# Optimization experiments

Measured on AMD Instinct MI355X. Metric: run time of the kernel, lower is better.

## Reference

```python
import jax, jax.numpy as jnp
import numpy as np

DIM = 64
K = 8
B_TAIL = 3.0
HIDDEN = 64
BATCH = 16384
MIN_BIN_WIDTH = 1e-3
MIN_BIN_HEIGHT = 1e-3
MIN_DERIVATIVE = 1e-3


def setup_inputs() -> dict:
    key = jax.random.key(0)
    ks = jax.random.split(key, 8)
    L = DIM - 1
    out_dim = 3 * K - 1
    def u(k, shape, fan_in):
        b = 1.0 / np.sqrt(fan_in)
        return jax.random.uniform(k, shape, minval=-b, maxval=b, dtype=jnp.float32)
    return {
        "x": jax.random.normal(ks[0], (BATCH, DIM), jnp.float32),
        "init_param": jax.random.uniform(ks[1], (out_dim,), minval=-0.5, maxval=0.5, dtype=jnp.float32),
        # conditioner MLP i (i=1..dim-1) maps x[:, :i] -> 3K-1; stacked with zero-masked inputs
        "W1": u(ks[2], (L, HIDDEN, DIM), DIM),
        "b1": u(ks[3], (L, HIDDEN), DIM),
        "W2": u(ks[4], (L, HIDDEN, HIDDEN), HIDDEN),
        "b2": u(ks[5], (L, HIDDEN), HIDDEN),
        "W3": u(ks[6], (L, out_dim, HIDDEN), HIDDEN),
        "b3": u(ks[7], (L, out_dim), HIDDEN),
    }


def _rqs(inputs, uW, uH, uD, left, right):
    # inputs: [D, B]; uW/uH: [D, B, K]; uD: [D, B, K+1] (already edge-padded)
    num_bins = uW.shape[-1]
    widths = jax.nn.softmax(uW, axis=-1)
    widths = MIN_BIN_WIDTH + (1 - MIN_BIN_WIDTH * num_bins) * widths
    cw = jnp.pad(jnp.cumsum(widths, axis=-1), ((0, 0), (0, 0), (1, 0)))
    cw = (right - left) * cw + left
    cw = cw.at[..., 0].set(left).at[..., -1].set(right)
    widths = cw[..., 1:] - cw[..., :-1]

    derivs = MIN_DERIVATIVE + jax.nn.softplus(uD)

    heights = jax.nn.softmax(uH, axis=-1)
    heights = MIN_BIN_HEIGHT + (1 - MIN_BIN_HEIGHT * num_bins) * heights
    ch = jnp.pad(jnp.cumsum(heights, axis=-1), ((0, 0), (0, 0), (1, 0)))
    ch = (right - left) * ch + left  # bottom=left, top=right (symmetric box)
    ch = ch.at[..., 0].set(left).at[..., -1].set(right)
    heights = ch[..., 1:] - ch[..., :-1]

    # searchsorted: sum(inputs >= bin_edges) - 1, with eps on last edge
    cw_s = cw.at[..., -1].add(1e-6)
    bin_idx = jnp.sum(inputs[..., None] >= cw_s, axis=-1) - 1
    bin_idx = jnp.clip(bin_idx, 0, num_bins - 1)[..., None]
    take = lambda a: jnp.take_along_axis(a, bin_idx, axis=-1)[..., 0]

    in_cw = take(cw)
    in_w = take(widths)
    in_ch = take(ch)
    in_h = take(heights)
    in_delta = take(heights / widths)
    d_k = take(derivs)
    d_k1 = take(derivs[..., 1:])

    theta = (inputs - in_cw) / in_w
    t1mt = theta * (1 - theta)
    numer = in_h * (in_delta * theta**2 + d_k * t1mt)
    denom = in_delta + (d_k + d_k1 - 2 * in_delta) * t1mt
    outputs = in_ch + numer / denom
    dnum = in_delta**2 * (d_k1 * theta**2 + 2 * in_delta * t1mt + d_k * (1 - theta) ** 2)
    logabsdet = jnp.log(dnum) - 2 * jnp.log(denom)
    return outputs, logabsdet


def _unconstrained_rqs(inputs, uW, uH, uD, tail_bound):
    inside = (inputs >= -tail_bound) & (inputs <= tail_bound)
    const = float(np.log(np.exp(1 - MIN_DERIVATIVE) - 1))
    uD = jnp.pad(uD, ((0, 0), (0, 0), (1, 1)), constant_values=const)
    x_in = jnp.clip(inputs, -tail_bound, tail_bound)
    out, ld = _rqs(x_in, uW, uH, uD, -tail_bound, tail_bound)
    return jnp.where(inside, out, inputs), jnp.where(inside, ld, 0.0)


def reference(x, init_param, W1, b1, W2, b2, W3, b3):
    Bsz = x.shape[0]
    L = DIM - 1
    # row l of mask keeps x[:, :l+1], zeroes the rest -> identical to per-layer x[:, :i]
    mask = jnp.tril(jnp.ones((L, DIM), x.dtype))
    xm = x[None, :, :] * mask[:, None, :]                         # [L, B, D]
    h = jnp.tanh(jnp.einsum('lbd,lhd->lbh', xm, W1) + b1[:, None, :])
    h = jnp.tanh(jnp.einsum('lbh,lgh->lbg', h, W2) + b2[:, None, :])
    out = jnp.einsum('lbh,loh->lbo', h, W3) + b3[:, None, :]      # [L, B, 3K-1]
    params = jnp.concatenate(
        [jnp.broadcast_to(init_param, (1, Bsz, 3 * K - 1)), out], axis=0)  # [D, B, 3K-1]
    W = 2 * B_TAIL * jax.nn.softmax(params[..., :K], axis=-1)
    H = 2 * B_TAIL * jax.nn.softmax(params[..., K:2 * K], axis=-1)
    Dp = jax.nn.softplus(params[..., 2 * K:])
    z_t, ld = _unconstrained_rqs(x.T, W, H, Dp, B_TAIL)           # [D, B]
    return z_t.T, ld.sum(axis=0)
```

## Files before the change

### kernel.cpp

```cpp
#include <hip/hip_runtime.h>

#define BATCH 16384
#define LAYERS 63
#define BM 128
#define XS 72
#define BLOB_BYTES 21504
#define LDS_OFF 8192
#define LDS_BYTES 13312

typedef float f4 __attribute__((ext_vector_type(4)));
typedef short s8 __attribute__((ext_vector_type(8)));
typedef unsigned int u4 __attribute__((ext_vector_type(4)));

#define LOG2E  1.442695041f
#define LN2    0.6931471806f

__device__ __forceinline__ float rcpf(float v) { return __builtin_amdgcn_rcpf(v); }

__device__ __forceinline__ float exp2_hw(float x) {
#if __has_builtin(__builtin_amdgcn_exp2f)
    return __builtin_amdgcn_exp2f(x);
#else
    return exp2f(x);
#endif
}

__device__ __forceinline__ float fast_tanh(float v) {
    float e = exp2_hw(v * (2.f * LOG2E));
    return 1.f - 2.f * rcpf(e + 1.f);
}
__device__ __forceinline__ float deriv_chain(float p) {
    return 1e-3f + LN2 * __log2f(2.f + exp2_hw(p * LOG2E));
}
__device__ __forceinline__ unsigned short f2bf(float f) {
    unsigned int u = __float_as_uint(f);
    u += 0x7fffu + ((u >> 16) & 1u);
    return (unsigned short)(u >> 16);
}
#if __has_builtin(__builtin_amdgcn_cvt_pk_bf16_f32)
__device__ __forceinline__ unsigned pk2(float a, float b) {
    auto r = __builtin_amdgcn_cvt_pk_bf16_f32(a, b);
    return __builtin_bit_cast(unsigned, r);
}
#else
__device__ __forceinline__ unsigned pk2(float a, float b) {
    return (unsigned)f2bf(a) | ((unsigned)f2bf(b) << 16);
}
#endif
__device__ __forceinline__ unsigned long long pack4(float a, float b, float c, float d) {
    return (unsigned long long)pk2(a, b) | ((unsigned long long)pk2(c, d) << 32);
}

__device__ __forceinline__ void rqs_eval(const float* p, float xv, float& zout, float& ldout) {
    const bool inside = (xv >= -3.f) && (xv <= 3.f);
    const float xi = fminf(fmaxf(xv, -3.f), 3.f);

    float wa[8], ha[8];
    {
        float s = 0.f;
        #pragma unroll
        for (int i = 0; i < 8; i++) { wa[i] = exp2_hw(p[i] * LOG2E); s += wa[i]; }
        float inv = 6.f * rcpf(s);
        #pragma unroll
        for (int i = 0; i < 8; i++) wa[i] *= inv;
        s = 0.f;
        #pragma unroll
        for (int i = 0; i < 8; i++) { wa[i] = exp2_hw(wa[i] * LOG2E); s += wa[i]; }
        inv = 0.992f * rcpf(s);
        #pragma unroll
        for (int i = 0; i < 8; i++) wa[i] = 1e-3f + wa[i] * inv;
    }
    {
        float s = 0.f;
        #pragma unroll
        for (int i = 0; i < 8; i++) { ha[i] = exp2_hw(p[8 + i] * LOG2E); s += ha[i]; }
        float inv = 6.f * rcpf(s);
        #pragma unroll
        for (int i = 0; i < 8; i++) ha[i] *= inv;
        s = 0.f;
        #pragma unroll
        for (int i = 0; i < 8; i++) { ha[i] = exp2_hw(ha[i] * LOG2E); s += ha[i]; }
        inv = 0.992f * rcpf(s);
        #pragma unroll
        for (int i = 0; i < 8; i++) ha[i] = 1e-3f + ha[i] * inv;
    }

    float cw[9], ch[9];
    cw[0] = -3.f; ch[0] = -3.f;
    {
        float cs = 0.f, hs = 0.f;
        #pragma unroll
        for (int k = 1; k < 8; k++) {
            cs += wa[k - 1]; cw[k] = 6.f * cs - 3.f;
            hs += ha[k - 1]; ch[k] = 6.f * hs - 3.f;
        }
    }
    cw[8] = 3.f; ch[8] = 3.f;

    int cnt = 0;
    #pragma unroll
    for (int k = 0; k < 8; k++) cnt += (xi >= cw[k]) ? 1 : 0;
    cnt += (xi >= 3.000001f) ? 1 : 0;
    const int bin = min(max(cnt - 1, 0), 7);

    float in_cw = 0.f, in_w = 1.f, in_ch = 0.f, in_h = 1.f;
    float pd0 = 0.f, pd1 = 0.f;
    #pragma unroll
    for (int k = 0; k < 8; k++)
        if (k == bin) {
            in_cw = cw[k]; in_w = cw[k + 1] - cw[k];
            in_ch = ch[k]; in_h = ch[k + 1] - ch[k];
            if (k >= 1) pd0 = p[15 + k];
            if (k <= 6) pd1 = p[16 + k];
        }
    const float dk  = (bin == 0) ? 1.f : deriv_chain(pd0);
    const float dk1 = (bin == 7) ? 1.f : deriv_chain(pd1);

    const float rw    = rcpf(in_w);
    const float delta = in_h * rw;
    const float th    = (xi - in_cw) * rw;
    const float omt = 1.f - th;
    const float t1  = th * omt;
    const float th2 = th * th;
    const float numer = in_h * (delta * th2 + dk * t1);
    const float denom = delta + (dk + dk1 - 2.f * delta) * t1;
    const float rd    = rcpf(denom);
    const float outv  = in_ch + numer * rd;
    const float dnum  = delta * delta * (dk1 * th2 + 2.f * delta * t1 + dk * omt * omt);
    const float ldv = LN2 * __log2f(dnum * rd * rd);

    zout  = inside ? outv : xv;
    ldout = inside ? ldv : 0.f;
}

__global__ __launch_bounds__(256) void prep_kernel(
    const float* __restrict__ x, const float* __restrict__ init_param,
    const float* __restrict__ W1, const float* __restrict__ W2, const float* __restrict__ W3,
    const float* __restrict__ b1, const float* __restrict__ b2, const float* __restrict__ b3,
    unsigned short* __restrict__ x_bf, unsigned char* __restrict__ blobG,
    float* __restrict__ z, float* __restrict__ ld)
{
    const int tid = threadIdx.x;
    if (blockIdx.x < 1024) {
        size_t idx = (size_t)blockIdx.x * 256 + tid;
        f4 v = *(const f4*)&x[idx * 4];
        *(unsigned long long*)&x_bf[idx * 4] = pack4(v[0], v[1], v[2], v[3]);
        return;
    }
    if (blockIdx.x >= 1024 + LAYERS) {
        const int row = (blockIdx.x - 1024 - LAYERS) * 256 + tid;
        float p[23];
        #pragma unroll
        for (int j = 0; j < 23; j++) p[j] = init_param[j];
        float zv, lv;
        rqs_eval(p, x[(size_t)row * 64], zv, lv);
        z[(size_t)row * 64] = zv;
        ld[row] = lv;
        return;
    }
    const int l = blockIdx.x - 1024;
    unsigned char* gb = blobG + (size_t)l * BLOB_BYTES;
    for (int e = tid; e < 1024; e += 256) {
        int m = e >> 9, r = (e >> 3) & 63, j = e & 7;
        const float* src = (m ? W2 : W1) + (size_t)l * 4096 + r * 64 + j * 8;
        unsigned long long lo = pack4(src[0], src[1], src[2], src[3]);
        unsigned long long hi = pack4(src[4], src[5], src[6], src[7]);
        unsigned long long* dst = (unsigned long long*)(gb + m * 8192 + r * 128 + ((j ^ (r & 7)) << 4));
        dst[0] = lo; dst[1] = hi;
    }
    if (tid < 256) {
        int r = tid >> 3, j = tid & 7;
        unsigned long long lo = 0ull, hi = 0ull;
        if (r < 23) {
            const float* src = W3 + (size_t)l * 1472 + r * 64 + j * 8;
            lo = pack4(src[0], src[1], src[2], src[3]);
            hi = pack4(src[4], src[5], src[6], src[7]);
        }
        unsigned long long* dst = (unsigned long long*)(gb + 16384 + r * 128 + ((j ^ (r & 7)) << 4));
        dst[0] = lo; dst[1] = hi;
    }
    if (tid < 64)        *(float*)(gb + 20480 + tid * 4)         = b1[l * 64 + tid];
    else if (tid < 128)  *(float*)(gb + 20736 + (tid - 64) * 4)  = b2[l * 64 + tid - 64];
    else if (tid < 160)  *(float*)(gb + 20992 + (tid - 128) * 4) = (tid - 128 < 23) ? b3[l * 23 + tid - 128] : 0.f;
    else                 { int e = tid - 160; if (e < 96) *(float*)(gb + 21120 + e * 4) = 0.f; }
}

__global__ __launch_bounds__(256, 5) void mlp_rqs_kernel(
    const float* __restrict__ x, const unsigned short* __restrict__ x_bf,
    const unsigned char* __restrict__ blobG,
    float* __restrict__ z, float* __restrict__ ld)
{
    const int l = blockIdx.y, keff = l + 1;
    const int b0 = blockIdx.x * BM;
    const int tid = threadIdx.x;
    const int ln = tid & 63, wv = tid >> 6;
    const int c = ln & 15, q = ln >> 4;
    const int mbase = wv * 32;
    const int c7 = c & 7;

    __shared__ __align__(16) unsigned char blob[LDS_BYTES];
    __shared__ __align__(16) unsigned short Hs[BM * XS];

    unsigned short* W2s = (unsigned short*)blob;
    unsigned short* W3s = (unsigned short*)(blob + 8192);
    const float* b1s = (const float*)(blob + 12288);
    const float* b2s = (const float*)(blob + 12544);
    const float* b3s = (const float*)(blob + 12800);
    float* PsF = (float*)Hs;

    const unsigned char* gblob = blobG + (size_t)l * BLOB_BYTES;

    for (int t = wv; t < 13; t += 4)
        __builtin_amdgcn_global_load_lds(
            (const __attribute__((address_space(1))) void*)(gblob + LDS_OFF + t * 1024 + ln * 16),
            (__attribute__((address_space(3))) void*)(blob + t * 1024 + ln * 16), 16, 0, 0);

    const int ks1 = (keff + 31) >> 5;

    s8 aw1[2][4];
    #pragma unroll
    for (int mt = 0; mt < 4; mt++)
        aw1[0][mt] = *(const s8*)(gblob + (mt * 16 + c) * 128 + ((q ^ c7) << 4));
    if (ks1 == 2) {
        #pragma unroll
        for (int mt = 0; mt < 4; mt++)
            aw1[1][mt] = *(const s8*)(gblob + (mt * 16 + c) * 128 + (((4 + q) ^ c7) << 4));
    }

    u4 B0u, B1u, B2u{}, B3u{};
    {
        const unsigned short* xr = x_bf + (size_t)(b0 + mbase + c) * 64 + q * 8;
        B0u = *(const u4*)xr;  B1u = *(const u4*)(xr + 1024);
        if (ks1 == 2) { B2u = *(const u4*)(xr + 32); B3u = *(const u4*)(xr + 1024 + 32); }
        const int n = keff - ((ks1 - 1) * 32 + q * 8);
        unsigned mk[4];
        #pragma unroll
        for (int i = 0; i < 4; i++) {
            int m = n - 2 * i;
            mk[i] = (m >= 2) ? 0xFFFFFFFFu : ((m == 1) ? 0xFFFFu : 0u);
        }
        if (ks1 == 2) {
            #pragma unroll
            for (int i = 0; i < 4; i++) { B2u[i] &= mk[i]; B3u[i] &= mk[i]; }
        } else {
            #pragma unroll
            for (int i = 0; i < 4; i++) { B0u[i] &= mk[i]; B1u[i] &= mk[i]; }
        }
    }
    const float xv = x[(size_t)(b0 + (tid & 127)) * 64 + keff];

    __syncthreads();

    {
        f4 acc[4][2];
        #pragma unroll
        for (int mt = 0; mt < 4; mt++) {
            f4 bv = *(const f4*)&b1s[mt * 16 + q * 4];
            acc[mt][0] = bv; acc[mt][1] = bv;
        }
        {
            s8 bx0 = __builtin_bit_cast(s8, B0u), bx1 = __builtin_bit_cast(s8, B1u);
            #pragma unroll
            for (int mt = 0; mt < 4; mt++) {
                acc[mt][0] = __builtin_amdgcn_mfma_f32_16x16x32_bf16(aw1[0][mt], bx0, acc[mt][0], 0, 0, 0);
                acc[mt][1] = __builtin_amdgcn_mfma_f32_16x16x32_bf16(aw1[0][mt], bx1, acc[mt][1], 0, 0, 0);
            }
        }
        if (ks1 == 2) {
            s8 bx0 = __builtin_bit_cast(s8, B2u), bx1 = __builtin_bit_cast(s8, B3u);
            #pragma unroll
            for (int mt = 0; mt < 4; mt++) {
                acc[mt][0] = __builtin_amdgcn_mfma_f32_16x16x32_bf16(aw1[1][mt], bx0, acc[mt][0], 0, 0, 0);
                acc[mt][1] = __builtin_amdgcn_mfma_f32_16x16x32_bf16(aw1[1][mt], bx1, acc[mt][1], 0, 0, 0);
            }
        }
        #pragma unroll
        for (int mt = 0; mt < 4; mt++)
            #pragma unroll
            for (int nt = 0; nt < 2; nt++) {
                f4 a = acc[mt][nt];
                unsigned long long w = (unsigned long long)pk2(fast_tanh(a[0]), fast_tanh(a[1]))
                    | ((unsigned long long)pk2(fast_tanh(a[2]), fast_tanh(a[3])) << 32);
                *(unsigned long long*)&Hs[(mbase + nt * 16 + c) * XS + mt * 16 + q * 4] = w;
            }
    }

    {
        f4 acc[4][2];
        #pragma unroll
        for (int mt = 0; mt < 4; mt++) {
            f4 bv = *(const f4*)&b2s[mt * 16 + q * 4];
            acc[mt][0] = bv; acc[mt][1] = bv;
        }
        #pragma unroll
        for (int ks = 0; ks < 2; ks++) {
            s8 bh0 = *(const s8*)&Hs[(mbase + c) * XS + ks * 32 + q * 8];
            s8 bh1 = *(const s8*)&Hs[(mbase + 16 + c) * XS + ks * 32 + q * 8];
            const int sb = ((ks * 4 + q) ^ c7) * 8;
            #pragma unroll
            for (int mt = 0; mt < 4; mt++) {
                s8 aw = *(const s8*)&W2s[(mt * 16 + c) * 64 + sb];
                acc[mt][0] = __builtin_amdgcn_mfma_f32_16x16x32_bf16(aw, bh0, acc[mt][0], 0, 0, 0);
                acc[mt][1] = __builtin_amdgcn_mfma_f32_16x16x32_bf16(aw, bh1, acc[mt][1], 0, 0, 0);
            }
        }
        #pragma unroll
        for (int mt = 0; mt < 4; mt++)
            #pragma unroll
            for (int nt = 0; nt < 2; nt++) {
                f4 a = acc[mt][nt];
                unsigned long long w = (unsigned long long)pk2(fast_tanh(a[0]), fast_tanh(a[1]))
                    | ((unsigned long long)pk2(fast_tanh(a[2]), fast_tanh(a[3])) << 32);
                *(unsigned long long*)&Hs[(mbase + nt * 16 + c) * XS + mt * 16 + q * 4] = w;
            }
    }

    {
        f4 acc3[2][2];
        #pragma unroll
        for (int mt = 0; mt < 2; mt++) {
            f4 bv = *(const f4*)&b3s[mt * 16 + q * 4];
            acc3[mt][0] = bv; acc3[mt][1] = bv;
        }
        #pragma unroll
        for (int ks = 0; ks < 2; ks++) {
            s8 bh0 = *(const s8*)&Hs[(mbase + c) * XS + ks * 32 + q * 8];
            s8 bh1 = *(const s8*)&Hs[(mbase + 16 + c) * XS + ks * 32 + q * 8];
            const int sb = ((ks * 4 + q) ^ c7) * 8;
            #pragma unroll
            for (int mt = 0; mt < 2; mt++) {
                s8 aw = *(const s8*)&W3s[(mt * 16 + c) * 64 + sb];
                acc3[mt][0] = __builtin_amdgcn_mfma_f32_16x16x32_bf16(aw, bh0, acc3[mt][0], 0, 0, 0);
                acc3[mt][1] = __builtin_amdgcn_mfma_f32_16x16x32_bf16(aw, bh1, acc3[mt][1], 0, 0, 0);
            }
        }
        #pragma unroll
        for (int mt = 0; mt < 2; mt++)
            #pragma unroll
            for (int nt = 0; nt < 2; nt++)
                *(f4*)&PsF[(mbase + nt * 16 + c) * 36 + mt * 16 + q * 4] = acc3[mt][nt];
    }
    __syncthreads();

    if (tid < BM) {
        const float* prow = &PsF[tid * 36];
        f4 pv0 = *(const f4*)(prow + 0);
        f4 pv1 = *(const f4*)(prow + 4);
        f4 pv2 = *(const f4*)(prow + 8);
        f4 pv3 = *(const f4*)(prow + 12);

        const bool inside = (xv >= -3.f) && (xv <= 3.f);
        const float xi = fminf(fmaxf(xv, -3.f), 3.f);

        float e[8];
        float s = 0.f;
        #pragma unroll
        for (int i = 0; i < 4; i++) { e[i]     = exp2_hw(pv0[i] * LOG2E); s += e[i]; }
        #pragma unroll
        for (int i = 0; i < 4; i++) { e[4 + i] = exp2_hw(pv1[i] * LOG2E); s += e[4 + i]; }
        float inv2 = (6.f * LOG2E) * rcpf(s);
        float s2 = 0.f;
        #pragma unroll
        for (int i = 0; i < 8; i++) { e[i] = exp2_hw(e[i] * inv2); s2 += e[i]; }
        float inv3 = (6.f * 0.992f) * rcpf(s2);

        float w6k  = 6e-3f + e[0] * inv3;
        float cs   = -3.f + w6k;
        float in_cw = -3.f, in_w = w6k;
        int bin = 0;
        #pragma unroll
        for (int k = 1; k < 8; k++) {
            w6k = 6e-3f + e[k] * inv3;
            const bool ge = (xi >= cs);
            in_cw = ge ? cs  : in_cw;
            in_w  = ge ? w6k : in_w;
            bin   = ge ? k   : bin;
            cs += w6k;
        }

        s = 0.f;
        #pragma unroll
        for (int i = 0; i < 4; i++) { e[i]     = exp2_hw(pv2[i] * LOG2E); s += e[i]; }
        #pragma unroll
        for (int i = 0; i < 4; i++) { e[4 + i] = exp2_hw(pv3[i] * LOG2E); s += e[4 + i]; }
        inv2 = (6.f * LOG2E) * rcpf(s);
        s2 = 0.f;
        #pragma unroll
        for (int i = 0; i < 8; i++) { e[i] = exp2_hw(e[i] * inv2); s2 += e[i]; }
        inv3 = (6.f * 0.992f) * rcpf(s2);

        float h6p = 6e-3f + e[0] * inv3;
        float csh = -3.f, in_ch = -3.f, in_h = h6p;
        #pragma unroll
        for (int k = 1; k < 8; k++) {
            csh += h6p;
            h6p = 6e-3f + e[k] * inv3;
            const bool sel = (bin >= k);
            in_ch = sel ? csh : in_ch;
            in_h  = sel ? h6p : in_h;
        }

        const float pd0 = prow[15 + bin];
        const float pd1 = prow[16 + bin];
        const float dk  = (bin == 0) ? 1.f : deriv_chain(pd0);
        const float dk1 = (bin == 7) ? 1.f : deriv_chain(pd1);

        const float rw    = rcpf(in_w);
        const float delta = in_h * rw;
        const float th    = (xi - in_cw) * rw;
        const float omt = 1.f - th;
        const float t1  = th * omt;
        const float th2 = th * th;
        const float numer = in_h * (delta * th2 + dk * t1);
        const float denom = delta + (dk + dk1 - 2.f * delta) * t1;
        const float rd    = rcpf(denom);
        const float outv  = in_ch + numer * rd;
        const float dnum  = delta * delta * (dk1 * th2 + 2.f * delta * t1 + dk * omt * omt);
        const float ldv = LN2 * __log2f(dnum * rd * rd);

        z[(size_t)(b0 + tid) * 64 + keff] = inside ? outv : xv;
        unsafeAtomicAdd(ld + b0 + tid, inside ? ldv : 0.f);
    }
}

extern "C" void kernel_launch(void* const* d_in, const int* in_sizes, int n_in,
                              void* d_out, int out_size, void* d_ws, size_t ws_size,
                              hipStream_t stream)
{
    const float* x  = (const float*)d_in[0];
    const float* ip = (const float*)d_in[1];
    const float* W1 = (const float*)d_in[2];
    const float* b1 = (const float*)d_in[3];
    const float* W2 = (const float*)d_in[4];
    const float* b2 = (const float*)d_in[5];
    const float* W3 = (const float*)d_in[6];
    const float* b3 = (const float*)d_in[7];

    float* z  = (float*)d_out;
    float* ld = z + (size_t)BATCH * 64;

    unsigned short* x_bf = (unsigned short*)d_ws;
    unsigned char*  blobG = (unsigned char*)(x_bf + (size_t)BATCH * 64);

    prep_kernel<<<1024 + LAYERS + 64, 256, 0, stream>>>(
        x, ip, W1, W2, W3, b1, b2, b3, x_bf, blobG, z, ld);
    mlp_rqs_kernel<<<dim3(BATCH / BM, LAYERS), 256, 0, stream>>>(
        x, x_bf, blobG, z, ld);
}
```

Baseline: 127.8 us.

## Use packed polynomial tanh and split the RQS epilogue across both thread halves

Replaces the exp-plus-reciprocal tanh with one exp2 of -|x| followed by a polynomial evaluated with packed two-wide FMAs, then restores the sign with copysign. This cuts transcendental instructions in the hidden-layer activations at the cost of more FMA work and some approximation error. The spline epilogue is also split. Threads 128-255, previously idle, now compute the height softmax and write the bin heights into spare LDS columns of each parameter row. Threads 0-127 compute widths, bin search and derivatives, then read the heights back after an added barrier.

```diff
diff --git a/kernel.cpp b/kernel.cpp
--- a/kernel.cpp
+++ b/kernel.cpp
@@ -9,6 +9,7 @@
 #define LDS_BYTES 13312
 
 typedef float f4 __attribute__((ext_vector_type(4)));
+typedef float f2 __attribute__((ext_vector_type(2)));
 typedef short s8 __attribute__((ext_vector_type(8)));
 typedef unsigned int u4 __attribute__((ext_vector_type(4)));
 
@@ -25,9 +26,22 @@
 #endif
 }
 
-__device__ __forceinline__ float fast_tanh(float v) {
-    float e = exp2_hw(v * (2.f * LOG2E));
-    return 1.f - 2.f * rcpf(e + 1.f);
+__device__ __forceinline__ f2 s2(float v) { return f2{v, v}; }
+
+__device__ __forceinline__ f2 tanh2(float x0, float x1) {
+    f2 u;
+    u[0] = exp2_hw(fabsf(x0) * -2.885390082f);
+    u[1] = exp2_hw(fabsf(x1) * -2.885390082f);
+    f2 q = __builtin_elementwise_fma(u, s2(-0.21528896f), s2(0.85191968f));
+    q = __builtin_elementwise_fma(q, u, s2(-1.55543360f));
+    q = __builtin_elementwise_fma(q, u, s2( 1.91204672f));
+    q = __builtin_elementwise_fma(q, u, s2(-1.99321600f));
+    q = __builtin_elementwise_fma(q, u, s2( 1.99991152f));
+    f2 r = __builtin_elementwise_fma(-q, u, s2(1.f));
+    f2 out;
+    out[0] = __builtin_copysignf(r[0], x0);
+    out[1] = __builtin_copysignf(r[1], x1);
+    return out;
 }
 __device__ __forceinline__ float deriv_chain(float p) {
     return 1e-3f + LN2 * __log2f(2.f + exp2_hw(p * LOG2E));
@@ -279,8 +293,9 @@
             #pragma unroll
             for (int nt = 0; nt < 2; nt++) {
                 f4 a = acc[mt][nt];
-                unsigned long long w = (unsigned long long)pk2(fast_tanh(a[0]), fast_tanh(a[1]))
-                    | ((unsigned long long)pk2(fast_tanh(a[2]), fast_tanh(a[3])) << 32);
+                f2 lo = tanh2(a[0], a[1]), hi = tanh2(a[2], a[3]);
+                unsigned long long w = (unsigned long long)pk2(lo[0], lo[1])
+                    | ((unsigned long long)pk2(hi[0], hi[1]) << 32);
                 *(unsigned long long*)&Hs[(mbase + nt * 16 + c) * XS + mt * 16 + q * 4] = w;
             }
     }
@@ -309,8 +324,9 @@
             #pragma unroll
             for (int nt = 0; nt < 2; nt++) {
                 f4 a = acc[mt][nt];
-                unsigned long long w = (unsigned long long)pk2(fast_tanh(a[0]), fast_tanh(a[1]))
-                    | ((unsigned long long)pk2(fast_tanh(a[2]), fast_tanh(a[3])) << 32);
+                f2 lo = tanh2(a[0], a[1]), hi = tanh2(a[2], a[3]);
+                unsigned long long w = (unsigned long long)pk2(lo[0], lo[1])
+                    | ((unsigned long long)pk2(hi[0], hi[1]) << 32);
                 *(unsigned long long*)&Hs[(mbase + nt * 16 + c) * XS + mt * 16 + q * 4] = w;
             }
     }
@@ -342,15 +358,37 @@
     }
     __syncthreads();
 
-    if (tid < BM) {
-        const float* prow = &PsF[tid * 36];
+    const int rrow = tid & 127;
+    float* prow = &PsF[rrow * 36];
+    float in_cw, in_w, xi, dk, dk1;
+    int bin = 0;
+    bool inside;
+
+    if (tid >= BM) {
+        f4 pv2 = *(const f4*)(prow + 8);
+        f4 pv3 = *(const f4*)(prow + 12);
+        float e[8];
+        float s = 0.f;
+        #pragma unroll
+        for (int i = 0; i < 4; i++) { e[i]     = exp2_hw(pv2[i] * LOG2E); s += e[i]; }
+        #pragma unroll
+        for (int i = 0; i < 4; i++) { e[4 + i] = exp2_hw(pv3[i] * LOG2E); s += e[4 + i]; }
+        float inv2 = (6.f * LOG2E) * rcpf(s);
+        float s2v = 0.f;
+        #pragma unroll
+        for (int i = 0; i < 8; i++) { e[i] = exp2_hw(e[i] * inv2); s2v += e[i]; }
+        float inv3 = (6.f * 0.992f) * rcpf(s2v);
+        f4 h0, h1;
+        #pragma unroll
+        for (int i = 0; i < 4; i++) { h0[i] = 6e-3f + e[i] * inv3; h1[i] = 6e-3f + e[4 + i] * inv3; }
+        *(f4*)(prow + 24) = h0;
+        *(f4*)(prow + 28) = h1;
+    } else {
         f4 pv0 = *(const f4*)(prow + 0);
         f4 pv1 = *(const f4*)(prow + 4);
-        f4 pv2 = *(const f4*)(prow + 8);
-        f4 pv3 = *(const f4*)(prow + 12);
-
-        const bool inside = (xv >= -3.f) && (xv <= 3.f);
-        const float xi = fminf(fmaxf(xv, -3.f), 3.f);
+
+        inside = (xv >= -3.f) && (xv <= 3.f);
+        xi = fminf(fmaxf(xv, -3.f), 3.f);
 
         float e[8];
         float s = 0.f;
@@ -359,15 +397,14 @@
         #pragma unroll
         for (int i = 0; i < 4; i++) { e[4 + i] = exp2_hw(pv1[i] * LOG2E); s += e[4 + i]; }
         float inv2 = (6.f * LOG2E) * rcpf(s);
-        float s2 = 0.f;
-        #pragma unroll
-        for (int i = 0; i < 8; i++) { e[i] = exp2_hw(e[i] * inv2); s2 += e[i]; }
-        float inv3 = (6.f * 0.992f) * rcpf(s2);
+        float s2v = 0.f;
+        #pragma unroll
+        for (int i = 0; i < 8; i++) { e[i] = exp2_hw(e[i] * inv2); s2v += e[i]; }
+        float inv3 = (6.f * 0.992f) * rcpf(s2v);
 
         float w6k  = 6e-3f + e[0] * inv3;
         float cs   = -3.f + w6k;
-        float in_cw = -3.f, in_w = w6k;
-        int bin = 0;
+        in_cw = -3.f; in_w = w6k;
         #pragma unroll
         for (int k = 1; k < 8; k++) {
             w6k = 6e-3f + e[k] * inv3;
@@ -378,32 +415,26 @@
             cs += w6k;
         }
 
-        s = 0.f;
-        #pragma unroll
-        for (int i = 0; i < 4; i++) { e[i]     = exp2_hw(pv2[i] * LOG2E); s += e[i]; }
-        #pragma unroll
-        for (int i = 0; i < 4; i++) { e[4 + i] = exp2_hw(pv3[i] * LOG2E); s += e[4 + i]; }
-        inv2 = (6.f * LOG2E) * rcpf(s);
-        s2 = 0.f;
-        #pragma unroll
-        for (int i = 0; i < 8; i++) { e[i] = exp2_hw(e[i] * inv2); s2 += e[i]; }
-        inv3 = (6.f * 0.992f) * rcpf(s2);
-
-        float h6p = 6e-3f + e[0] * inv3;
-        float csh = -3.f, in_ch = -3.f, in_h = h6p;
-        #pragma unroll
-        for (int k = 1; k < 8; k++) {
-            csh += h6p;
-            h6p = 6e-3f + e[k] * inv3;
-            const bool sel = (bin >= k);
-            in_ch = sel ? csh : in_ch;
-            in_h  = sel ? h6p : in_h;
-        }
-
         const float pd0 = prow[15 + bin];
         const float pd1 = prow[16 + bin];
-        const float dk  = (bin == 0) ? 1.f : deriv_chain(pd0);
-        const float dk1 = (bin == 7) ? 1.f : deriv_chain(pd1);
+        dk  = (bin == 0) ? 1.f : deriv_chain(pd0);
+        dk1 = (bin == 7) ? 1.f : deriv_chain(pd1);
+    }
+    __syncthreads();
+
+    if (tid < BM) {
+        f4 h6a = *(const f4*)(prow + 24);
+        f4 h6b = *(const f4*)(prow + 28);
+        float h6[8] = {h6a[0], h6a[1], h6a[2], h6a[3], h6b[0], h6b[1], h6b[2], h6b[3]};
+
+        float csh = -3.f, in_ch = -3.f, in_h = h6[0];
+        #pragma unroll
+        for (int k = 1; k < 8; k++) {
+            csh += h6[k - 1];
+            const bool sel = (bin >= k);
+            in_ch = sel ? csh   : in_ch;
+            in_h  = sel ? h6[k] : in_h;
+        }
 
         const float rw    = rcpf(in_w);
         const float delta = in_h * rw;
```

After: 132.5 us. +3.7%, slower.
